# Kernel tuning notes

Measured on AMD Instinct MI355X. Metric: run time of the kernel, lower is better.

Reference implementation:

```python
import jax, jax.numpy as jnp
import numpy as np

B, T, N, NL, DIM, H, DH = 8, 8, 1024, 64, 1024, 16, 64
HID = H * DH
SCALE = np.float32(np.sqrt(DH))  # note: divides the POST-softmax probs (faithful to source)


def _layernorm(x, g, b, eps=1e-5):
    m = jnp.mean(x, axis=-1, keepdims=True)
    v = jnp.mean(jnp.square(x - m), axis=-1, keepdims=True)
    return (x - m) / jnp.sqrt(v + eps) * g + b


def setup_inputs() -> dict:
    key = jax.random.key(0)
    ks = jax.random.split(key, 5)
    s = 0.02
    return {
        "media": jax.random.normal(ks[0], (B, T, N, DIM), jnp.float32),
        "latents": jax.random.normal(ks[1], (B, T, NL, DIM), jnp.float32),
        "g_m": jnp.ones((DIM,), jnp.float32),
        "b_m": jnp.zeros((DIM,), jnp.float32),
        "g_l": jnp.ones((DIM,), jnp.float32),
        "b_l": jnp.zeros((DIM,), jnp.float32),
        "Wq": jax.random.normal(ks[2], (DIM, HID), jnp.float32) * s,
        "Wkv": jax.random.normal(ks[3], (DIM, 2 * HID), jnp.float32) * s,
        "Wout": jax.random.normal(ks[4], (HID, DIM), jnp.float32) * s,
    }


def reference(media, latents, g_m, b_m, g_l, b_l, Wq, Wkv, Wout):
    media = _layernorm(media, g_m, b_m)      # [B,T,N,DIM]
    latents = _layernorm(latents, g_l, b_l)  # [B,T,NL,DIM]
    kv_in = jnp.concatenate([media, latents], axis=-2)  # [B,T,N+NL,DIM]
    q = (latents @ Wq).reshape(B, T, NL, H, DH)
    kv = kv_in @ Wkv
    k, v = jnp.split(kv, 2, axis=-1)
    k = k.reshape(B, T, N + NL, H, DH)
    v = v.reshape(B, T, N + NL, H, DH)
    attn = jnp.einsum('btqhd,btkhd->bhtqk', q, k)  # [B,H,T,NL,N+NL]
    attn = attn - jax.lax.stop_gradient(jnp.max(attn, axis=-1, keepdims=True))
    p = jax.nn.softmax(attn, axis=-1) / SCALE      # unusual post-softmax scale
    out = jnp.einsum('bhtqk,btkhd->btqhd', p, v).reshape(B, T, NL, HID)
    return out @ Wout
```

## Files before the change

### kernel.cpp

```cpp
#include <hip/hip_runtime.h>


typedef __attribute__((ext_vector_type(8))) short s8v;
typedef __attribute__((ext_vector_type(4))) float f4v;

#define BT_ 64
#define NKV 1088
#define NKV_PAD 1152

__device__ __forceinline__ ushort f2bf(float f){
  union { float f; unsigned u; } v; v.f = f;
  unsigned r = v.u + 0x7FFFu + ((v.u >> 16) & 1u);
  return (ushort)(r >> 16);
}

__device__ __forceinline__ void gload_lds16(const ushort* g, ushort* l){
  __builtin_amdgcn_global_load_lds((const __attribute__((address_space(1))) void*)g,
                                   (__attribute__((address_space(3))) void*)l,
                                   16, 0, 0);
}

__device__ __forceinline__ int xcd_swizzle(int orig, int nwg){
  int q = nwg >> 3, r = nwg & 7;
  int xcd = orig & 7, idx = orig >> 3;
  return (xcd < r ? xcd*(q+1) : r*(q+1) + (xcd-r)*q) + idx;
}

__global__ __launch_bounds__(256)
void ln_kernel(const float* __restrict__ media, const float* __restrict__ latents,
               const float* __restrict__ g_m, const float* __restrict__ b_m,
               const float* __restrict__ g_l, const float* __restrict__ b_l,
               ushort* __restrict__ lnA){
  int g = blockIdx.x;
  int bt = g / 1088, rr = g - bt * 1088;
  const float* src; const float* gam; const float* bet;
  if (rr < 1024){ src = media   + ((long)bt*1024 + rr)        *1024; gam = g_m; bet = b_m; }
  else          { src = latents + ((long)bt*64   + (rr-1024)) *1024; gam = g_l; bet = b_l; }
  int tid = threadIdx.x;
  float4 x = ((const float4*)src)[tid];
  float s  = x.x + x.y + x.z + x.w;
  float s2 = x.x*x.x + x.y*x.y + x.z*x.z + x.w*x.w;
  #pragma unroll
  for (int off = 32; off > 0; off >>= 1){
    s  += __shfl_down(s,  off);
    s2 += __shfl_down(s2, off);
  }
  __shared__ float ps[4], ps2[4];
  if ((tid & 63) == 0){ ps[tid>>6] = s; ps2[tid>>6] = s2; }
  __syncthreads();
  float tot  = ps[0]+ps[1]+ps[2]+ps[3];
  float tot2 = ps2[0]+ps2[1]+ps2[2]+ps2[3];
  float mean = tot * (1.f/1024.f);
  float var  = tot2 * (1.f/1024.f) - mean*mean;
  float rinv = rsqrtf(var + 1e-5f);
  float4 gm4 = ((const float4*)gam)[tid];
  float4 bt4 = ((const float4*)bet)[tid];
  ushort4 o;
  o.x = f2bf((x.x-mean)*rinv*gm4.x + bt4.x);
  o.y = f2bf((x.y-mean)*rinv*gm4.y + bt4.y);
  o.z = f2bf((x.z-mean)*rinv*gm4.z + bt4.z);
  o.w = f2bf((x.w-mean)*rinv*gm4.w + bt4.w);
  *(ushort4*)&lnA[((long)bt*NKV_PAD + rr)*1024 + tid*4] = o;
}

__global__ __launch_bounds__(256)
void transpose_cast(const float* __restrict__ W, ushort* __restrict__ WT, int K, int N){
  __shared__ float tile[32][33];
  int n0 = blockIdx.x*32, k0 = blockIdx.y*32;
  int tx = threadIdx.x & 31, ty = threadIdx.x >> 5;
  #pragma unroll
  for (int i = 0; i < 32; i += 8) tile[ty+i][tx] = W[(long)(k0+ty+i)*N + n0+tx];
  __syncthreads();
  #pragma unroll
  for (int i = 0; i < 32; i += 8) WT[(long)(n0+ty+i)*K + k0+tx] = f2bf(tile[tx][ty+i]);
}

template<int STORE_BF16>
__global__ __launch_bounds__(256)
void gemm_tn(const ushort* __restrict__ A, long strideAbatch,
             const ushort* __restrict__ BT,
             void* __restrict__ C, long strideCbatch,
             int Mvalid, int N, int tiles_n, int tiles_per_batch){
  constexpr int K = 1024;
  __shared__ ushort As[128*32];
  __shared__ ushort Bs[128*32];
  int wgid = xcd_swizzle(blockIdx.x, gridDim.x);
  int batch = wgid / tiles_per_batch;
  int tile  = wgid - batch*tiles_per_batch;
  int tm = tile / tiles_n, tn = tile % tiles_n;
  const ushort* Ab = A  + (long)batch*strideAbatch + (long)tm*128*K;
  const ushort* Bb = BT + (long)tn*128*K;
  int tid = threadIdx.x;
  int lane = tid & 63, wave = tid >> 6;
  int wm = wave >> 1, wn = wave & 1;
  f4v acc[4][4] = {};

  for (int kt = 0; kt < K/32; ++kt){
    #pragma unroll
    for (int r = 0; r < 4; ++r){
      int slot = r*256 + tid;
      const ushort* g; ushort* l;
      if (slot < 512){
        int row = slot >> 2, seg = slot & 3;
        g = Ab + (long)row*K + kt*32 + seg*8;
        l = &As[(r*256 + wave*64)*8];
      } else {
        int s2 = slot - 512;
        int row = s2 >> 2, seg = s2 & 3;
        g = Bb + (long)row*K + kt*32 + seg*8;
        l = &Bs[((r-2)*256 + wave*64)*8];
      }
      gload_lds16(g, l);
    }
    __syncthreads();
    s8v av[4], bv[4];
    #pragma unroll
    for (int m = 0; m < 4; ++m)
      av[m] = *(const s8v*)&As[(wm*64 + m*16 + (lane&15))*32 + (lane>>4)*8];
    #pragma unroll
    for (int n = 0; n < 4; ++n)
      bv[n] = *(const s8v*)&Bs[(wn*64 + n*16 + (lane&15))*32 + (lane>>4)*8];
    #pragma unroll
    for (int m = 0; m < 4; ++m)
      #pragma unroll
      for (int n = 0; n < 4; ++n)
        acc[m][n] = __builtin_amdgcn_mfma_f32_16x16x32_bf16(av[m], bv[n], acc[m][n], 0, 0, 0);
    __syncthreads();
  }

  long cb = (long)batch*strideCbatch;
  #pragma unroll
  for (int m = 0; m < 4; ++m){
    int row0 = tm*128 + wm*64 + m*16 + ((lane>>4)<<2);
    #pragma unroll
    for (int n = 0; n < 4; ++n){
      int col = tn*128 + wn*64 + n*16 + (lane&15);
      #pragma unroll
      for (int j = 0; j < 4; ++j){
        int row = row0 + j;
        if (row < Mvalid){
          if (STORE_BF16) ((ushort*)C)[cb + (long)row*N + col] = f2bf(acc[m][n][j]);
          else            ((float*) C)[cb + (long)row*N + col] = acc[m][n][j];
        }
      }
    }
  }
}

__global__ __launch_bounds__(256)
void attn_kernel(const ushort* __restrict__ qbuf, const ushort* __restrict__ kv,
                 ushort* __restrict__ aout){
  __shared__ ushort Qs [64*72];
  __shared__ ushort Ks [64*72];
  __shared__ ushort VTs[64*72];
  __shared__ ushort Ps [64*72];
  int blk = xcd_swizzle(blockIdx.x, gridDim.x);
  int bt = blk >> 4, h = blk & 15;
  int tid = threadIdx.x, lane = tid & 63, wave = tid >> 6;

  {
    int r = tid >> 2, c0 = (tid & 3) * 16;
    const ushort* src = &qbuf[((long)bt*64 + r)*1024 + h*64 + c0];
    *(s8v*)&Qs[r*72 + c0]     = *(const s8v*)(src);
    *(s8v*)&Qs[r*72 + c0 + 8] = *(const s8v*)(src + 8);
  }
  float m_[4], l_[4];
  f4v accO[4] = {};
  #pragma unroll
  for (int j = 0; j < 4; ++j){ m_[j] = -1e30f; l_[j] = 0.f; }
  const long kvbase = (long)bt*NKV*2048;

  for (int t0 = 0; t0 < NKV; t0 += 64){
    __syncthreads();
    {
      int r = tid >> 2, c0 = (tid & 3) * 16;
      const ushort* src = &kv[kvbase + (long)(t0+r)*2048 + h*64 + c0];
      *(s8v*)&Ks[r*72 + c0]     = *(const s8v*)(src);
      *(s8v*)&Ks[r*72 + c0 + 8] = *(const s8v*)(src + 8);
    }
    {
      int kk = tid & 63, dg = tid >> 6;
      s8v v0 = *(const s8v*)&kv[kvbase + (long)(t0+kk)*2048 + 1024 + h*64 + dg*16];
      s8v v1 = *(const s8v*)&kv[kvbase + (long)(t0+kk)*2048 + 1024 + h*64 + dg*16 + 8];
      #pragma unroll
      for (int e = 0; e < 8; ++e) VTs[(dg*16+e)  *72 + kk] = v0[e];
      #pragma unroll
      for (int e = 0; e < 8; ++e) VTs[(dg*16+8+e)*72 + kk] = v1[e];
    }
    __syncthreads();

    f4v s[4] = {};
    s8v aq0 = *(const s8v*)&Qs[(wave*16 + (lane&15))*72 +      (lane>>4)*8];
    s8v aq1 = *(const s8v*)&Qs[(wave*16 + (lane&15))*72 + 32 + (lane>>4)*8];
    #pragma unroll
    for (int n = 0; n < 4; ++n){
      s8v bk0 = *(const s8v*)&Ks[(n*16 + (lane&15))*72 +      (lane>>4)*8];
      s8v bk1 = *(const s8v*)&Ks[(n*16 + (lane&15))*72 + 32 + (lane>>4)*8];
      s[n] = __builtin_amdgcn_mfma_f32_16x16x32_bf16(aq0, bk0, s[n], 0, 0, 0);
      s[n] = __builtin_amdgcn_mfma_f32_16x16x32_bf16(aq1, bk1, s[n], 0, 0, 0);
    }

    #pragma unroll
    for (int j = 0; j < 4; ++j){
      float v = fmaxf(fmaxf(s[0][j], s[1][j]), fmaxf(s[2][j], s[3][j]));
      #pragma unroll
      for (int off = 1; off < 16; off <<= 1) v = fmaxf(v, __shfl_xor(v, off));
      float mn = fmaxf(m_[j], v);
      float sc = __expf(m_[j] - mn);
      m_[j] = mn;
      float ss = 0.f;
      #pragma unroll
      for (int n = 0; n < 4; ++n){ float pv = __expf(s[n][j] - mn); s[n][j] = pv; ss += pv; }
      #pragma unroll
      for (int off = 1; off < 16; off <<= 1) ss += __shfl_xor(ss, off);
      l_[j] = l_[j]*sc + ss;
      #pragma unroll
      for (int dn = 0; dn < 4; ++dn) accO[dn][j] *= sc;
    }

    #pragma unroll
    for (int n = 0; n < 4; ++n)
      #pragma unroll
      for (int j = 0; j < 4; ++j)
        Ps[(wave*16 + ((lane>>4)<<2) + j)*72 + n*16 + (lane&15)] = f2bf(s[n][j]);

    s8v pa0 = *(const s8v*)&Ps[(wave*16 + (lane&15))*72 +      (lane>>4)*8];
    s8v pa1 = *(const s8v*)&Ps[(wave*16 + (lane&15))*72 + 32 + (lane>>4)*8];
    #pragma unroll
    for (int dn = 0; dn < 4; ++dn){
      s8v bv0 = *(const s8v*)&VTs[(dn*16 + (lane&15))*72 +      (lane>>4)*8];
      s8v bv1 = *(const s8v*)&VTs[(dn*16 + (lane&15))*72 + 32 + (lane>>4)*8];
      accO[dn] = __builtin_amdgcn_mfma_f32_16x16x32_bf16(pa0, bv0, accO[dn], 0, 0, 0);
      accO[dn] = __builtin_amdgcn_mfma_f32_16x16x32_bf16(pa1, bv1, accO[dn], 0, 0, 0);
    }
  }

  #pragma unroll
  for (int dn = 0; dn < 4; ++dn)
    #pragma unroll
    for (int j = 0; j < 4; ++j){
      int q = wave*16 + ((lane>>4)<<2) + j;
      float o = accO[dn][j] / (l_[j] * 8.0f);
      aout[((long)bt*128 + q)*1024 + h*64 + dn*16 + (lane&15)] = f2bf(o);
    }
}

static constexpr size_t SZ_LNA   = (size_t)BT_*NKV_PAD*1024*2;
static constexpr size_t SZ_KV    = (size_t)BT_*NKV*2048*2;
static constexpr size_t SZ_Q     = (size_t)BT_*64*1024*2;
static constexpr size_t SZ_AO    = (size_t)BT_*128*1024*2;
static constexpr size_t SZ_WQT   = (size_t)1024*1024*2;
static constexpr size_t SZ_WKVT  = (size_t)2048*1024*2;

extern "C" void kernel_launch(void* const* d_in, const int* in_sizes, int n_in,
                              void* d_out, int out_size, void* d_ws, size_t ws_size,
                              hipStream_t stream){
  const float* media   = (const float*)d_in[0];
  const float* latents = (const float*)d_in[1];
  const float* g_m     = (const float*)d_in[2];
  const float* b_m     = (const float*)d_in[3];
  const float* g_l     = (const float*)d_in[4];
  const float* b_l     = (const float*)d_in[5];
  const float* Wq      = (const float*)d_in[6];
  const float* Wkv     = (const float*)d_in[7];
  const float* Wout    = (const float*)d_in[8];

  char* ws = (char*)d_ws;
  ushort* lnA   = (ushort*)(ws);
  ushort* kvb   = (ushort*)(ws + SZ_LNA);
  ushort* qb    = (ushort*)(ws + SZ_LNA + SZ_KV);
  ushort* aob   = (ushort*)(ws + SZ_LNA + SZ_KV + SZ_Q);
  ushort* WqT   = (ushort*)(ws + SZ_LNA + SZ_KV + SZ_Q + SZ_AO);
  ushort* WkvT  = (ushort*)(ws + SZ_LNA + SZ_KV + SZ_Q + SZ_AO + SZ_WQT);
  ushort* WoutT = (ushort*)(ws + SZ_LNA + SZ_KV + SZ_Q + SZ_AO + SZ_WQT + SZ_WKVT);

  ln_kernel<<<BT_*1088, 256, 0, stream>>>(media, latents, g_m, b_m, g_l, b_l, lnA);
  transpose_cast<<<dim3(1024/32, 1024/32), 256, 0, stream>>>(Wq,   WqT,   1024, 1024);
  transpose_cast<<<dim3(2048/32, 1024/32), 256, 0, stream>>>(Wkv,  WkvT,  1024, 2048);
  transpose_cast<<<dim3(1024/32, 1024/32), 256, 0, stream>>>(Wout, WoutT, 1024, 1024);

  gemm_tn<1><<<9*16*BT_, 256, 0, stream>>>(lnA, (long)NKV_PAD*1024, WkvT,
                                           kvb, (long)NKV*2048, NKV, 2048, 16, 9*16);
  gemm_tn<1><<<8*BT_, 256, 0, stream>>>(lnA + 1024*1024, (long)NKV_PAD*1024, WqT,
                                        qb, (long)64*1024, 64, 1024, 8, 8);

  attn_kernel<<<BT_*16, 256, 0, stream>>>(qb, kvb, aob);

  gemm_tn<0><<<8*BT_, 256, 0, stream>>>(aob, (long)128*1024, WoutT,
                                        d_out, (long)64*1024, 64, 1024, 8, 8);
}
```

Before: 965.6 us.

## Add 256x256 pipelined KV GEMM writing transposed V, prefetch K/V in attention

Replaces the 128x128 KV projection GEMM with a 256x256-tile, 512-thread kernel. It uses double-buffered swizzled LDS staging via global_load_lds, interleaved MFMA phases with setprio, and row clamping, which removes the padded lnA layout. The V half is written pre-transposed per head, so the attention kernel loads V with plain vector copies instead of a scalar LDS transpose, and it register-prefetches the next K/V tile. The cost is a large 128KB dynamic LDS footprint and complex hand-scheduled waitcnt logic that could hide correctness bugs.

```diff
diff --git a/kernel.cpp b/kernel.cpp
--- a/kernel.cpp
+++ b/kernel.cpp
@@ -6,7 +6,6 @@
 
 #define BT_ 64
 #define NKV 1088
-#define NKV_PAD 1152
 
 __device__ __forceinline__ ushort f2bf(float f){
   union { float f; unsigned u; } v; v.f = f;
@@ -60,7 +59,7 @@
   o.y = f2bf((x.y-mean)*rinv*gm4.y + bt4.y);
   o.z = f2bf((x.z-mean)*rinv*gm4.z + bt4.z);
   o.w = f2bf((x.w-mean)*rinv*gm4.w + bt4.w);
-  *(ushort4*)&lnA[((long)bt*NKV_PAD + rr)*1024 + tid*4] = o;
+  *(ushort4*)&lnA[((long)bt*1088 + rr)*1024 + tid*4] = o;
 }
 
 __global__ __launch_bounds__(256)
@@ -75,10 +74,147 @@
   for (int i = 0; i < 32; i += 8) WT[(long)(n0+ty+i)*K + k0+tx] = f2bf(tile[tx][ty+i]);
 }
 
+#define MFMAQ(MH, NH, AF, BF) \
+  _Pragma("unroll") for (int m_ = 0; m_ < 4; ++m_){ \
+  _Pragma("unroll") for (int n_ = 0; n_ < 2; ++n_){ \
+    acc[(MH)*4+m_][(NH)*2+n_] = __builtin_amdgcn_mfma_f32_16x16x32_bf16(AF[m_*2+0], BF[n_*2+0], acc[(MH)*4+m_][(NH)*2+n_], 0,0,0); \
+    acc[(MH)*4+m_][(NH)*2+n_] = __builtin_amdgcn_mfma_f32_16x16x32_bf16(AF[m_*2+1], BF[n_*2+1], acc[(MH)*4+m_][(NH)*2+n_], 0,0,0); } }
+
+#define READA(DST, BUFB, MH) \
+  _Pragma("unroll") for (int m_ = 0; m_ < 4; ++m_){ \
+  _Pragma("unroll") for (int ks_ = 0; ks_ < 2; ++ks_){ \
+    int R_ = wm*128 + (MH)*64 + m_*16 + l15; \
+    DST[m_*2+ks_] = *(const s8v*)((BUFB) + R_*64 + (((ks_*64 + cB) ^ ((R_&7)<<4))>>1)); } }
+
+#define READB(DST, BUFB, NH) \
+  _Pragma("unroll") for (int n_ = 0; n_ < 2; ++n_){ \
+  _Pragma("unroll") for (int ks_ = 0; ks_ < 2; ++ks_){ \
+    int R_ = wn*64 + (NH)*32 + n_*16 + l15; \
+    DST[n_*2+ks_] = *(const s8v*)((BUFB) + R_*64 + (((ks_*64 + cB) ^ ((R_&7)<<4))>>1)); } }
+
+#define PHASE_TAIL(MH, NH, AF, BF) \
+  __builtin_amdgcn_s_barrier(); \
+  __builtin_amdgcn_s_setprio(1); \
+  MFMAQ(MH, NH, AF, BF); \
+  __builtin_amdgcn_s_setprio(0); \
+  asm volatile("s_waitcnt lgkmcnt(0)" ::: "memory"); \
+  __builtin_amdgcn_s_barrier();
+
+__global__ __launch_bounds__(512, 2)
+void gemm256_kv(const ushort* __restrict__ lnA, const ushort* __restrict__ WkvT,
+                ushort* __restrict__ kvK, ushort* __restrict__ VT){
+  extern __shared__ ushort smem[];
+  ushort* As = smem;
+  ushort* Bs = smem + 32768;
+
+  int wgid = xcd_swizzle(blockIdx.x, gridDim.x);
+  int batch = wgid / 40;
+  int rem   = wgid - batch*40;
+  int tm = rem >> 3, tn = rem & 7;
+
+  const ushort* Ab = lnA + (size_t)batch*1088*1024;
+  const ushort* Bb = WkvT;
+
+  int tid = threadIdx.x;
+  int lane = tid & 63, wave = tid >> 6;
+  int wm = wave >> 2, wn = wave & 3;
+  int l15 = lane & 15, cB = (lane >> 4) * 16;
+
+  auto STAGE = [&](const ushort* gbase, int grow0, int clampR, ushort* lds){
+    #pragma unroll
+    for (int rnd = 0; rnd < 2; ++rnd){
+      int idx = rnd*512 + tid;
+      int row = idx >> 3;
+      int colB = (idx & 7) << 4;
+      int lcol = colB ^ ((row & 7) << 4);
+      int gr = grow0 + row; gr = gr > clampR ? clampR : gr;
+      gload_lds16(gbase + (size_t)gr*1024 + (lcol >> 1), lds + idx*8);
+    }
+  };
+
+  f4v acc[8][4] = {};
+  s8v aF0[8], aF1[8], bF0[4], bF1[4];
+
+  STAGE(Ab,      tm*256,       1087, As);
+  STAGE(Ab,      tm*256 + 128, 1087, As + 8192);
+  STAGE(Bb,      tn*256,       2047, Bs);
+  STAGE(Bb,      tn*256 + 128, 2047, Bs + 8192);
+  STAGE(Ab + 64, tm*256,       1087, As + 16384);
+  STAGE(Ab + 64, tm*256 + 128, 1087, As + 16384 + 8192);
+  asm volatile("s_waitcnt vmcnt(4)" ::: "memory");
+  __builtin_amdgcn_s_barrier();
+
+  for (int i = 0; i < 8; ++i){
+    int k1 = 2*i + 1, k2 = 2*i + 2, k3 = 2*i + 3;
+    READA(aF0, As, 0)
+    READB(bF0, Bs, 0)
+    STAGE(Bb + k1*64, tn*256, 2047, Bs + 16384);
+    PHASE_TAIL(0, 0, aF0, bF0)
+    READA(aF1, As, 1)
+    STAGE(Bb + k1*64, tn*256 + 128, 2047, Bs + 16384 + 8192);
+    PHASE_TAIL(1, 0, aF1, bF0)
+    READB(bF1, Bs, 1)
+    if (k2 < 16) STAGE(Ab + k2*64, tm*256, 1087, As);
+    PHASE_TAIL(0, 1, aF0, bF1)
+    if (k2 < 16) STAGE(Ab + k2*64, tm*256 + 128, 1087, As + 8192);
+    if (i < 7) asm volatile("s_waitcnt vmcnt(4)" ::: "memory");
+    else       asm volatile("s_waitcnt vmcnt(0)" ::: "memory");
+    PHASE_TAIL(1, 1, aF1, bF1)
+    READA(aF0, As + 16384, 0)
+    READB(bF0, Bs + 16384, 0)
+    if (k2 < 16) STAGE(Bb + k2*64, tn*256, 2047, Bs);
+    PHASE_TAIL(0, 0, aF0, bF0)
+    READA(aF1, As + 16384, 1)
+    if (k2 < 16) STAGE(Bb + k2*64, tn*256 + 128, 2047, Bs + 8192);
+    PHASE_TAIL(1, 0, aF1, bF0)
+    READB(bF1, Bs + 16384, 1)
+    if (k3 < 16) STAGE(Ab + k3*64, tm*256, 1087, As + 16384);
+    PHASE_TAIL(0, 1, aF0, bF1)
+    if (k3 < 16) STAGE(Ab + k3*64, tm*256 + 128, 1087, As + 16384 + 8192);
+    if (i < 7) asm volatile("s_waitcnt vmcnt(4)" ::: "memory");
+    else       asm volatile("s_waitcnt vmcnt(0)" ::: "memory");
+    PHASE_TAIL(1, 1, aF1, bF1)
+  }
+
+  int colbase = tn*256 + wn*64;
+  if (tn < 4){
+    ushort* outp = kvK + (size_t)batch*1088*1024;
+    #pragma unroll
+    for (int m = 0; m < 8; ++m){
+      int row0 = tm*256 + wm*128 + m*16 + ((lane>>4)<<2);
+      #pragma unroll
+      for (int n = 0; n < 4; ++n){
+        int col = colbase + n*16 + l15;
+        #pragma unroll
+        for (int j = 0; j < 4; ++j){
+          int row = row0 + j;
+          if (row < 1088) outp[(size_t)row*1024 + col] = f2bf(acc[m][n][j]);
+        }
+      }
+    }
+  } else {
+    #pragma unroll
+    for (int m = 0; m < 8; ++m){
+      int kk0 = tm*256 + wm*128 + m*16 + ((lane>>4)<<2);
+      if (kk0 < 1088){
+        #pragma unroll
+        for (int n = 0; n < 4; ++n){
+          int col = colbase - 1024 + n*16 + l15;
+          int h = col >> 6, dh = col & 63;
+          ushort4 o;
+          o.x = f2bf(acc[m][n][0]); o.y = f2bf(acc[m][n][1]);
+          o.z = f2bf(acc[m][n][2]); o.w = f2bf(acc[m][n][3]);
+          *(ushort4*)&VT[(((size_t)batch*16 + h)*64 + dh)*1088 + kk0] = o;
+        }
+      }
+    }
+  }
+}
+
 template<int STORE_BF16>
 __global__ __launch_bounds__(256)
-void gemm_tn(const ushort* __restrict__ A, long strideAbatch,
-             const ushort* __restrict__ BT,
+void gemm_tn(const ushort* __restrict__ A, long strideAbatch, int clampRel,
+             const ushort* __restrict__ BTm,
              void* __restrict__ C, long strideCbatch,
              int Mvalid, int N, int tiles_n, int tiles_per_batch){
   constexpr int K = 1024;
@@ -89,7 +225,7 @@
   int tile  = wgid - batch*tiles_per_batch;
   int tm = tile / tiles_n, tn = tile % tiles_n;
   const ushort* Ab = A  + (long)batch*strideAbatch + (long)tm*128*K;
-  const ushort* Bb = BT + (long)tn*128*K;
+  const ushort* Bb = BTm + (long)tn*128*K;
   int tid = threadIdx.x;
   int lane = tid & 63, wave = tid >> 6;
   int wm = wave >> 1, wn = wave & 1;
@@ -102,6 +238,7 @@
       const ushort* g; ushort* l;
       if (slot < 512){
         int row = slot >> 2, seg = slot & 3;
+        if (row > clampRel) row = clampRel;
         g = Ab + (long)row*K + kt*32 + seg*8;
         l = &As[(r*256 + wave*64)*8];
       } else {
@@ -148,18 +285,18 @@
 }
 
 __global__ __launch_bounds__(256)
-void attn_kernel(const ushort* __restrict__ qbuf, const ushort* __restrict__ kv,
-                 ushort* __restrict__ aout){
+void attn_kernel(const ushort* __restrict__ qbuf, const ushort* __restrict__ kvK,
+                 const ushort* __restrict__ VT, ushort* __restrict__ aout){
   __shared__ ushort Qs [64*72];
   __shared__ ushort Ks [64*72];
-  __shared__ ushort VTs[64*72];
+  __shared__ ushort Vs [64*72];
   __shared__ ushort Ps [64*72];
   int blk = xcd_swizzle(blockIdx.x, gridDim.x);
   int bt = blk >> 4, h = blk & 15;
   int tid = threadIdx.x, lane = tid & 63, wave = tid >> 6;
+  int r = tid >> 2, c0 = (tid & 3) * 16;
 
   {
-    int r = tid >> 2, c0 = (tid & 3) * 16;
     const ushort* src = &qbuf[((long)bt*64 + r)*1024 + h*64 + c0];
     *(s8v*)&Qs[r*72 + c0]     = *(const s8v*)(src);
     *(s8v*)&Qs[r*72 + c0 + 8] = *(const s8v*)(src + 8);
@@ -168,24 +305,29 @@
   f4v accO[4] = {};
   #pragma unroll
   for (int j = 0; j < 4; ++j){ m_[j] = -1e30f; l_[j] = 0.f; }
-  const long kvbase = (long)bt*NKV*2048;
-
-  for (int t0 = 0; t0 < NKV; t0 += 64){
+  const long kbase = (long)bt*1088*1024;
+  const long vbase = ((long)bt*16 + h)*64*1088;
+
+  s8v kr0, kr1, vr0, vr1;
+  {
+    const ushort* ks = &kvK[kbase + (long)r*1024 + h*64 + c0];
+    kr0 = *(const s8v*)(ks); kr1 = *(const s8v*)(ks + 8);
+    const ushort* vs = &VT[vbase + (long)r*1088 + c0];
+    vr0 = *(const s8v*)(vs); vr1 = *(const s8v*)(vs + 8);
+  }
+
+  for (int it = 0; it < 17; ++it){
+    int t0 = it * 64;
     __syncthreads();
-    {
-      int r = tid >> 2, c0 = (tid & 3) * 16;
-      const ushort* src = &kv[kvbase + (long)(t0+r)*2048 + h*64 + c0];
-      *(s8v*)&Ks[r*72 + c0]     = *(const s8v*)(src);
-      *(s8v*)&Ks[r*72 + c0 + 8] = *(const s8v*)(src + 8);
-    }
-    {
-      int kk = tid & 63, dg = tid >> 6;
-      s8v v0 = *(const s8v*)&kv[kvbase + (long)(t0+kk)*2048 + 1024 + h*64 + dg*16];
-      s8v v1 = *(const s8v*)&kv[kvbase + (long)(t0+kk)*2048 + 1024 + h*64 + dg*16 + 8];
-      #pragma unroll
-      for (int e = 0; e < 8; ++e) VTs[(dg*16+e)  *72 + kk] = v0[e];
-      #pragma unroll
-      for (int e = 0; e < 8; ++e) VTs[(dg*16+8+e)*72 + kk] = v1[e];
+    *(s8v*)&Ks[r*72 + c0]     = kr0;
+    *(s8v*)&Ks[r*72 + c0 + 8] = kr1;
+    *(s8v*)&Vs[r*72 + c0]     = vr0;
+    *(s8v*)&Vs[r*72 + c0 + 8] = vr1;
+    if (it + 1 < 17){
+      const ushort* ks = &kvK[kbase + (long)(t0+64+r)*1024 + h*64 + c0];
+      kr0 = *(const s8v*)(ks); kr1 = *(const s8v*)(ks + 8);
+      const ushort* vs = &VT[vbase + (long)r*1088 + t0+64 + c0];
+      vr0 = *(const s8v*)(vs); vr1 = *(const s8v*)(vs + 8);
     }
     __syncthreads();
 
@@ -228,8 +370,8 @@
     s8v pa1 = *(const s8v*)&Ps[(wave*16 + (lane&15))*72 + 32 + (lane>>4)*8];
     #pragma unroll
     for (int dn = 0; dn < 4; ++dn){
-      s8v bv0 = *(const s8v*)&VTs[(dn*16 + (lane&15))*72 +      (lane>>4)*8];
-      s8v bv1 = *(const s8v*)&VTs[(dn*16 + (lane&15))*72 + 32 + (lane>>4)*8];
+      s8v bv0 = *(const s8v*)&Vs[(dn*16 + (lane&15))*72 +      (lane>>4)*8];
+      s8v bv1 = *(const s8v*)&Vs[(dn*16 + (lane&15))*72 + 32 + (lane>>4)*8];
       accO[dn] = __builtin_amdgcn_mfma_f32_16x16x32_bf16(pa0, bv0, accO[dn], 0, 0, 0);
       accO[dn] = __builtin_amdgcn_mfma_f32_16x16x32_bf16(pa1, bv1, accO[dn], 0, 0, 0);
     }
@@ -245,12 +387,13 @@
     }
 }
 
-static constexpr size_t SZ_LNA   = (size_t)BT_*NKV_PAD*1024*2;
-static constexpr size_t SZ_KV    = (size_t)BT_*NKV*2048*2;
-static constexpr size_t SZ_Q     = (size_t)BT_*64*1024*2;
-static constexpr size_t SZ_AO    = (size_t)BT_*128*1024*2;
-static constexpr size_t SZ_WQT   = (size_t)1024*1024*2;
-static constexpr size_t SZ_WKVT  = (size_t)2048*1024*2;
+static constexpr size_t SZ_LNA = (size_t)BT_*1088*1024*2;
+static constexpr size_t SZ_KVK = (size_t)BT_*1088*1024*2;
+static constexpr size_t SZ_VT  = (size_t)BT_*16*64*1088*2;
+static constexpr size_t SZ_Q   = (size_t)BT_*64*1024*2;
+static constexpr size_t SZ_AO  = (size_t)BT_*128*1024*2;
+static constexpr size_t SZ_WQT = (size_t)1024*1024*2;
+static constexpr size_t SZ_WKVT= (size_t)2048*1024*2;
 
 extern "C" void kernel_launch(void* const* d_in, const int* in_sizes, int n_in,
                               void* d_out, int out_size, void* d_ws, size_t ws_size,
@@ -267,25 +410,28 @@
 
   char* ws = (char*)d_ws;
   ushort* lnA   = (ushort*)(ws);
-  ushort* kvb   = (ushort*)(ws + SZ_LNA);
-  ushort* qb    = (ushort*)(ws + SZ_LNA + SZ_KV);
-  ushort* aob   = (ushort*)(ws + SZ_LNA + SZ_KV + SZ_Q);
-  ushort* WqT   = (ushort*)(ws + SZ_LNA + SZ_KV + SZ_Q + SZ_AO);
-  ushort* WkvT  = (ushort*)(ws + SZ_LNA + SZ_KV + SZ_Q + SZ_AO + SZ_WQT);
-  ushort* WoutT = (ushort*)(ws + SZ_LNA + SZ_KV + SZ_Q + SZ_AO + SZ_WQT + SZ_WKVT);
+  ushort* kvK   = (ushort*)(ws + SZ_LNA);
+  ushort* VT    = (ushort*)(ws + SZ_LNA + SZ_KVK);
+  ushort* qb    = (ushort*)(ws + SZ_LNA + SZ_KVK + SZ_VT);
+  ushort* aob   = (ushort*)(ws + SZ_LNA + SZ_KVK + SZ_VT + SZ_Q);
+  ushort* WqT   = (ushort*)(ws + SZ_LNA + SZ_KVK + SZ_VT + SZ_Q + SZ_AO);
+  ushort* WkvT  = (ushort*)(ws + SZ_LNA + SZ_KVK + SZ_VT + SZ_Q + SZ_AO + SZ_WQT);
+  ushort* WoutT = (ushort*)(ws + SZ_LNA + SZ_KVK + SZ_VT + SZ_Q + SZ_AO + SZ_WQT + SZ_WKVT);
 
   ln_kernel<<<BT_*1088, 256, 0, stream>>>(media, latents, g_m, b_m, g_l, b_l, lnA);
   transpose_cast<<<dim3(1024/32, 1024/32), 256, 0, stream>>>(Wq,   WqT,   1024, 1024);
   transpose_cast<<<dim3(2048/32, 1024/32), 256, 0, stream>>>(Wkv,  WkvT,  1024, 2048);
   transpose_cast<<<dim3(1024/32, 1024/32), 256, 0, stream>>>(Wout, WoutT, 1024, 1024);
 
-  gemm_tn<1><<<9*16*BT_, 256, 0, stream>>>(lnA, (long)NKV_PAD*1024, WkvT,
-                                           kvb, (long)NKV*2048, NKV, 2048, 16, 9*16);
-  gemm_tn<1><<<8*BT_, 256, 0, stream>>>(lnA + 1024*1024, (long)NKV_PAD*1024, WqT,
+  hipFuncSetAttribute((const void*)gemm256_kv,
+                      hipFuncAttributeMaxDynamicSharedMemorySize, 131072);
+  gemm256_kv<<<2560, 512, 131072, stream>>>(lnA, WkvT, kvK, VT);
+
+  gemm_tn<1><<<8*BT_, 256, 0, stream>>>(lnA + 1024*1024, (long)1088*1024, 63, WqT,
                                         qb, (long)64*1024, 64, 1024, 8, 8);
 
-  attn_kernel<<<BT_*16, 256, 0, stream>>>(qb, kvb, aob);
-
-  gemm_tn<0><<<8*BT_, 256, 0, stream>>>(aob, (long)128*1024, WoutT,
+  attn_kernel<<<BT_*16, 256, 0, stream>>>(qb, kvK, VT, aob);
+
+  gemm_tn<0><<<8*BT_, 256, 0, stream>>>(aob, (long)128*1024, 127, WoutT,
                                         d_out, (long)64*1024, 64, 1024, 8, 8);
 }
```

Result: slower. 1.037 ms (+7.4%).
